# Kernel optimization log

Measured on AMD Instinct MI355X. Metric: run time of the kernel, lower is better.

Reference implementation:

```python
import jax, jax.numpy as jnp
import numpy as np

D_MODEL = 1024
N_HEADS = 16
D_K = D_MODEL // N_HEADS


def setup_inputs() -> dict:
    key = jax.random.key(0)
    ks = jax.random.split(key, 5)
    s = 1.0 / np.sqrt(D_MODEL)
    x = jax.random.normal(ks[0], (4, 2048, D_MODEL), dtype=jnp.float32)
    W_qkv = jax.random.normal(ks[1], (D_MODEL, 3 * D_MODEL), dtype=jnp.float32) * s
    b_qkv = jnp.zeros((3 * D_MODEL,), dtype=jnp.float32)
    W_proj = jax.random.normal(ks[2], (D_MODEL, D_MODEL), dtype=jnp.float32) * s
    b_proj = jnp.zeros((D_MODEL,), dtype=jnp.float32)
    return {"x": x, "W_qkv": W_qkv, "b_qkv": b_qkv, "W_proj": W_proj, "b_proj": b_proj}


def reference(x, W_qkv, b_qkv, W_proj, b_proj):
    B, T, C = x.shape
    qkv = x @ W_qkv + b_qkv  # [B,T,3C]
    q, k, v = jnp.split(qkv, 3, axis=2)
    # [B,T,C] -> [B,H,T,dk]
    def to_heads(t):
        return t.reshape(B, T, N_HEADS, D_K).transpose(0, 2, 1, 3)
    q, k, v = to_heads(q), to_heads(k), to_heads(v)
    scale = 1.0 / np.sqrt(D_K)
    att = jnp.einsum('bhqd,bhkd->bhqk', q, k) * scale
    causal = jnp.tril(jnp.ones((T, T), dtype=bool))
    att = jnp.where(causal, att, -jnp.inf)
    att = jax.nn.softmax(att, axis=-1)
    y = jnp.einsum('bhqk,bhkd->bhqd', att, v)
    y = y.transpose(0, 2, 1, 3).reshape(B, T, C)
    return y @ W_proj + b_proj
```

## Files before the change

kernel.cpp:

```cpp
#include <hip/hip_runtime.h>
#include <stdint.h>


typedef float  floatx4  __attribute__((ext_vector_type(4)));
typedef float  f32x16   __attribute__((ext_vector_type(16)));
typedef __bf16 bf16x8   __attribute__((ext_vector_type(8)));
typedef __bf16 bf16x4   __attribute__((ext_vector_type(4)));
typedef unsigned int u32;
typedef u32    u32x4    __attribute__((ext_vector_type(4)));

#define AS1 __attribute__((address_space(1)))
#define AS3 __attribute__((address_space(3)))

__device__ __forceinline__ void gload_lds16(const void* g, void* l) {
    __builtin_amdgcn_global_load_lds((AS1 void*)(uintptr_t)g,
                                     (AS3 void*)(uintptr_t)l, 16, 0, 0);
}

#if __has_builtin(__builtin_amdgcn_exp2f)
#define EXP2F(x) __builtin_amdgcn_exp2f(x)
#else
#define EXP2F(x) exp2f(x)
#endif

__device__ __forceinline__ u32 pkbf(float lo, float hi) {
    union { __bf16 h[2]; u32 u; } x;
    x.h[0] = (__bf16)lo; x.h[1] = (__bf16)hi;
    return x.u;
}

__device__ __forceinline__ void plswap(u32& a, u32& b) {
    asm volatile("v_permlane32_swap_b32 %0, %1" : "+v"(a), "+v"(b));
}

#define LOG2E 1.44269504088896340736f
#define ATT_SC (0.125f * LOG2E)
#define MASK_NEG (-3.0e4f)

static constexpr int Bn = 4, Tn = 2048, Cn = 1024, Hn = 16, DKn = 64;
static constexpr int BT = Bn * Tn;
static constexpr int N_QKV = 3 * Cn;
static constexpr int KPAD = 66;
static constexpr int VPAD = 130;


__global__ void cast_x_kernel(const float* __restrict__ x, __bf16* __restrict__ xb, int n) {
    int i = (blockIdx.x * blockDim.x + threadIdx.x) * 4;
    if (i < n) {
        float4 v = *(const float4*)(x + i);
        bf16x4 o;
        o[0] = (__bf16)v.x; o[1] = (__bf16)v.y; o[2] = (__bf16)v.z; o[3] = (__bf16)v.w;
        *(bf16x4*)(xb + i) = o;
    }
}

__global__ void transpose_cast_kernel(const float* __restrict__ W, __bf16* __restrict__ WT,
                                      int R, int C) {
    __shared__ float tile[32][33];
    int tx = threadIdx.x & 31, ty = threadIdx.x >> 5;
    int r0 = blockIdx.y * 32, c0 = blockIdx.x * 32;
#pragma unroll
    for (int i = 0; i < 4; i++)
        tile[ty + i * 8][tx] = W[(size_t)(r0 + ty + i * 8) * C + c0 + tx];
    __syncthreads();
#pragma unroll
    for (int i = 0; i < 4; i++)
        WT[(size_t)(c0 + ty + i * 8) * R + r0 + tx] = (__bf16)tile[tx][ty + i * 8];
}

__device__ __forceinline__ void xcd_swizzle(int gx, int* bn, int* bm) {
    int flat = blockIdx.y * gx + blockIdx.x;
    int nwg = gx * gridDim.y;
    int cpx = nwg >> 3;
    int swz = (flat & 7) * cpx + (flat >> 3);
    *bm = swz / gx;
    *bn = swz - *bm * gx;
}

__global__ __launch_bounds__(256) void gemm_qkv_kernel(
    const __bf16* __restrict__ A, const __bf16* __restrict__ Bt,
    const float* __restrict__ bias,
    __bf16* __restrict__ Qo, __bf16* __restrict__ Ko, __bf16* __restrict__ Vo) {
    const int K = 1024;
    __shared__ __bf16 Al[128 * 64];
    __shared__ __bf16 Bl[128 * 64];
    int tid = threadIdx.x, w = tid >> 6, lane = tid & 63;
    int lq = lane >> 4, l16 = lane & 15;
    int bm, bn;
    xcd_swizzle(gridDim.x, &bn, &bm);
    int wm = w & 1, wn = w >> 1;

    int srow = lane >> 3;
    int scb  = (lane & 7) ^ (srow & 7);
    const __bf16* Ag = A + (size_t)(bm * 128 + w * 32 + srow) * K + scb * 8;
    const __bf16* Bg = Bt + (size_t)(bn * 128 + w * 32 + srow) * K + scb * 8;
    __bf16* AlW = Al + w * 32 * 64;
    __bf16* BlW = Bl + w * 32 * 64;

    const int co0 = ((0 * 4 + lq) ^ (l16 & 7)) * 8;
    const int co1 = ((1 * 4 + lq) ^ (l16 & 7)) * 8;

    floatx4 acc[4][4] = {};
    for (int k0 = 0; k0 < K; k0 += 64) {
        __syncthreads();
#pragma unroll
        for (int c = 0; c < 4; c++) {
            gload_lds16(Ag + k0 + (size_t)c * 8 * K, AlW + c * 8 * 64);
            gload_lds16(Bg + k0 + (size_t)c * 8 * K, BlW + c * 8 * 64);
        }
        __syncthreads();
#pragma unroll
        for (int ks = 0; ks < 2; ks++) {
            const int co = ks ? co1 : co0;
            bf16x8 af[4], bf[4];
#pragma unroll
            for (int i = 0; i < 4; i++)
                af[i] = *(const bf16x8*)&Al[(wm * 64 + i * 16 + l16) * 64 + co];
#pragma unroll
            for (int i = 0; i < 4; i++)
                bf[i] = *(const bf16x8*)&Bl[(wn * 64 + i * 16 + l16) * 64 + co];
#pragma unroll
            for (int mt = 0; mt < 4; mt++)
#pragma unroll
                for (int nt = 0; nt < 4; nt++)
                    acc[mt][nt] = __builtin_amdgcn_mfma_f32_16x16x32_bf16(
                        af[mt], bf[nt], acc[mt][nt], 0, 0, 0);
        }
    }
#pragma unroll
    for (int nt = 0; nt < 4; nt++) {
        int gbase = bn * 128 + wn * 64 + nt * 16;
        int gcol = gbase + l16;
        int which = gbase >> 10;
        float bv = bias[gcol];
        if (which == 2) {
            int hh = (gbase - 2048) >> 6;
            int dd = ((gbase - 2048) & 63) + l16;
#pragma unroll
            for (int mt = 0; mt < 4; mt++) {
                int growb = bm * 128 + wm * 64 + mt * 16 + lq * 4;
                int bb = growb >> 11, tt = growb & 2047;
                bf16x4 v4;
#pragma unroll
                for (int r = 0; r < 4; r++) v4[r] = (__bf16)(acc[mt][nt][r] + bv);
                *(bf16x4*)&Vo[((size_t)(bb * 16 + hh) * 64 + dd) * 2048 + tt] = v4;
            }
        } else {
            int rem = gbase & 1023;
            int hh = rem >> 6, dd = (rem & 63) + l16;
            __bf16* dst = (which == 0) ? Qo : Ko;
            float scl = (which == 0) ? ATT_SC : 1.0f;
#pragma unroll
            for (int mt = 0; mt < 4; mt++) {
#pragma unroll
                for (int r = 0; r < 4; r++) {
                    int grow = bm * 128 + wm * 64 + mt * 16 + lq * 4 + r;
                    int bb = grow >> 11, tt = grow & 2047;
                    dst[((size_t)(bb * 16 + hh) * 2048 + tt) * 64 + dd] =
                        (__bf16)((acc[mt][nt][r] + bv) * scl);
                }
            }
        }
    }
}

__global__ __launch_bounds__(256) void gemm_proj_kernel(
    const __bf16* __restrict__ A, const __bf16* __restrict__ Bt,
    const float* __restrict__ bias, float* __restrict__ out) {
    const int K = 1024;
    __shared__ __bf16 Al[128 * 64];
    __shared__ __bf16 Bl[128 * 64];
    int tid = threadIdx.x, w = tid >> 6, lane = tid & 63;
    int lq = lane >> 4, l16 = lane & 15;
    int bm, bn;
    xcd_swizzle(gridDim.x, &bn, &bm);
    int wm = w & 1, wn = w >> 1;

    int srow = lane >> 3;
    int scb  = (lane & 7) ^ (srow & 7);
    const __bf16* Ag = A + (size_t)(bm * 128 + w * 32 + srow) * K + scb * 8;
    const __bf16* Bg = Bt + (size_t)(bn * 128 + w * 32 + srow) * K + scb * 8;
    __bf16* AlW = Al + w * 32 * 64;
    __bf16* BlW = Bl + w * 32 * 64;

    const int co0 = ((0 * 4 + lq) ^ (l16 & 7)) * 8;
    const int co1 = ((1 * 4 + lq) ^ (l16 & 7)) * 8;

    floatx4 acc[4][4] = {};
    for (int k0 = 0; k0 < K; k0 += 64) {
        __syncthreads();
#pragma unroll
        for (int c = 0; c < 4; c++) {
            gload_lds16(Ag + k0 + (size_t)c * 8 * K, AlW + c * 8 * 64);
            gload_lds16(Bg + k0 + (size_t)c * 8 * K, BlW + c * 8 * 64);
        }
        __syncthreads();
#pragma unroll
        for (int ks = 0; ks < 2; ks++) {
            const int co = ks ? co1 : co0;
            bf16x8 af[4], bf[4];
#pragma unroll
            for (int i = 0; i < 4; i++)
                af[i] = *(const bf16x8*)&Al[(wm * 64 + i * 16 + l16) * 64 + co];
#pragma unroll
            for (int i = 0; i < 4; i++)
                bf[i] = *(const bf16x8*)&Bl[(wn * 64 + i * 16 + l16) * 64 + co];
#pragma unroll
            for (int mt = 0; mt < 4; mt++)
#pragma unroll
                for (int nt = 0; nt < 4; nt++)
                    acc[mt][nt] = __builtin_amdgcn_mfma_f32_16x16x32_bf16(
                        af[mt], bf[nt], acc[mt][nt], 0, 0, 0);
        }
    }
#pragma unroll
    for (int nt = 0; nt < 4; nt++) {
        int gcol = bn * 128 + wn * 64 + nt * 16 + l16;
        float bv = bias[gcol];
#pragma unroll
        for (int mt = 0; mt < 4; mt++) {
#pragma unroll
            for (int r = 0; r < 4; r++) {
                int grow = bm * 128 + wm * 64 + mt * 16 + lq * 4 + r;
                out[(size_t)grow * 1024 + gcol] = acc[mt][nt][r] + bv;
            }
        }
    }
}

__global__ __launch_bounds__(256) void attn_kernel(
    const __bf16* __restrict__ Q, const __bf16* __restrict__ K,
    const __bf16* __restrict__ Vt, __bf16* __restrict__ Y) {
    const int bid = blockIdx.x;
    const int pr = bid >> 6, bh = bid & 63;
    const int b = bh >> 4, h = bh & 15;
    int tid = threadIdx.x, w = tid >> 6, lane = tid & 63;
    int l32 = lane & 31, hi = lane >> 5;

    const __bf16* Qh = Q + (size_t)bh * Tn * DKn;
    const __bf16* Kh = K + (size_t)bh * Tn * DKn;
    const __bf16* Vh = Vt + (size_t)bh * DKn * Tn;

    __shared__ __bf16 Kl[128 * KPAD];
    __shared__ __bf16 Vl[64 * VPAD];

    int skrow = tid >> 3, sksl = tid & 7;
    int svrow = tid >> 4, svsl = tid & 15;

    bf16x8 kr[4], vr[4];
#pragma unroll
    for (int i = 0; i < 4; i++) {
        kr[i] = *(const bf16x8*)&Kh[(size_t)(skrow + i * 32) * 64 + sksl * 8];
        vr[i] = *(const bf16x8*)&Vh[(size_t)(svrow + i * 16) * 2048 + svsl * 8];
    }

#pragma unroll
    for (int seg = 0; seg < 2; seg++) {
        const int qt = seg ? (15 - pr) : pr;
        const int q0 = qt * 128;
        const int ktmax = qt;
        const int qrow = q0 + w * 32 + l32;

        bf16x8 qf[4];
#pragma unroll
        for (int ds = 0; ds < 4; ds++)
            qf[ds] = *(const bf16x8*)&Qh[(size_t)qrow * 64 + ds * 16 + hi * 8];

        f32x16 oacc0 = {}, oacc1 = {};
        float rs = 0.0f;

        for (int kt = 0; kt <= ktmax; kt++) {
            __syncthreads();
#pragma unroll
            for (int i = 0; i < 4; i++) {
                *(bf16x8*)&Kl[(skrow + i * 32) * KPAD + sksl * 8] = kr[i];
                *(bf16x8*)&Vl[(svrow + i * 16) * VPAD + svsl * 8] = vr[i];
            }
            __syncthreads();
            if (!(seg == 1 && kt == ktmax)) {
                int nk = (kt < ktmax) ? (kt + 1) : 0;
#pragma unroll
                for (int i = 0; i < 4; i++) {
                    kr[i] = *(const bf16x8*)&Kh[(size_t)(nk * 128 + skrow + i * 32) * 64 + sksl * 8];
                    vr[i] = *(const bf16x8*)&Vh[(size_t)(svrow + i * 16) * 2048 + nk * 128 + svsl * 8];
                }
            }

#pragma unroll
            for (int ktile = 0; ktile < 4; ktile++) {
                f32x16 s = {};
#pragma unroll
                for (int ds = 0; ds < 4; ds++) {
                    bf16x8 ka = *(const bf16x8*)&Kl[(ktile * 32 + l32) * KPAD +
                                                    ds * 16 + hi * 8];
                    s = __builtin_amdgcn_mfma_f32_32x32x16_bf16(ka, qf[ds], s, 0, 0, 0);
                }

                if (kt == qt) {
                    int kbase = kt * 128 + ktile * 32 + 4 * hi;
#pragma unroll
                    for (int r = 0; r < 16; r++) {
                        int key = kbase + (r & 3) + 8 * (r >> 2);
                        if (key > qrow) s[r] = MASK_NEG;
                    }
                }

                u32 G0a, G0b, G1a, G1b, G2a, G2b, G3a, G3b;
                {
                    float p0 = EXP2F(s[0]),  p1 = EXP2F(s[1]),  p2 = EXP2F(s[2]),  p3 = EXP2F(s[3]);
                    float p4 = EXP2F(s[4]),  p5 = EXP2F(s[5]),  p6 = EXP2F(s[6]),  p7 = EXP2F(s[7]);
                    float p8 = EXP2F(s[8]),  p9 = EXP2F(s[9]),  pa = EXP2F(s[10]), pb_ = EXP2F(s[11]);
                    float pc = EXP2F(s[12]), pd = EXP2F(s[13]), pe = EXP2F(s[14]), pf = EXP2F(s[15]);
                    rs += (((p0 + p1) + (p2 + p3)) + ((p4 + p5) + (p6 + p7))) +
                          (((p8 + p9) + (pa + pb_)) + ((pc + pd) + (pe + pf)));
                    G0a = pkbf(p0, p1);  G0b = pkbf(p2, p3);
                    G1a = pkbf(p4, p5);  G1b = pkbf(p6, p7);
                    G2a = pkbf(p8, p9);  G2b = pkbf(pa, pb_);
                    G3a = pkbf(pc, pd);  G3b = pkbf(pe, pf);
                }

#pragma unroll
                for (int t = 0; t < 2; t++) {
                    u32 a0 = t ? G2a : G0a, b0 = t ? G3a : G1a;
                    u32 a1 = t ? G2b : G0b, b1 = t ? G3b : G1b;
                    plswap(a0, b0);
                    plswap(a1, b1);
                    u32x4 wv = {a0, a1, b0, b1};
                    bf16x8 pbf = __builtin_bit_cast(bf16x8, wv);

                    int kc = ktile * 32 + t * 16 + hi * 8;
                    bf16x8 va0 = *(const bf16x8*)&Vl[(0 * 32 + l32) * VPAD + kc];
                    bf16x8 va1 = *(const bf16x8*)&Vl[(1 * 32 + l32) * VPAD + kc];
                    oacc0 = __builtin_amdgcn_mfma_f32_32x32x16_bf16(va0, pbf, oacc0, 0, 0, 0);
                    oacc1 = __builtin_amdgcn_mfma_f32_32x32x16_bf16(va1, pbf, oacc1, 0, 0, 0);
                }
            }
        }

        float tot = rs + __shfl_xor(rs, 32);
        float inv = 1.0f / tot;
#pragma unroll
        for (int dt2 = 0; dt2 < 2; dt2++) {
#pragma unroll
            for (int rg = 0; rg < 4; rg++) {
                bf16x4 v4;
#pragma unroll
                for (int e = 0; e < 4; e++) {
                    float o = dt2 ? oacc1[rg * 4 + e] : oacc0[rg * 4 + e];
                    v4[e] = (__bf16)(o * inv);
                }
                int d = dt2 * 32 + 8 * rg + 4 * hi;
                *(bf16x4*)&Y[((size_t)(b * 2048 + qrow)) * 1024 + h * 64 + d] = v4;
            }
        }
    }
}


extern "C" void kernel_launch(void* const* d_in, const int* in_sizes, int n_in,
                              void* d_out, int out_size, void* d_ws, size_t ws_size,
                              hipStream_t stream) {
    const float* x     = (const float*)d_in[0];
    const float* Wqkv  = (const float*)d_in[1];
    const float* bqkv  = (const float*)d_in[2];
    const float* Wproj = (const float*)d_in[3];
    const float* bproj = (const float*)d_in[4];
    float* out = (float*)d_out;

    __bf16* xb     = (__bf16*)d_ws;
    __bf16* WqkvT  = xb + (size_t)BT * Cn;
    __bf16* WprojT = WqkvT + (size_t)N_QKV * Cn;
    __bf16* Qb     = WprojT + (size_t)Cn * Cn;
    __bf16* Kb     = Qb + (size_t)BT * Cn;
    __bf16* Vb     = Kb + (size_t)BT * Cn;
    __bf16* Yb     = Vb + (size_t)BT * Cn;

    int nx = BT * Cn;
    cast_x_kernel<<<(nx / 4 + 255) / 256, 256, 0, stream>>>(x, xb, nx);
    transpose_cast_kernel<<<dim3(N_QKV / 32, Cn / 32), 256, 0, stream>>>(Wqkv, WqkvT, Cn, N_QKV);
    transpose_cast_kernel<<<dim3(Cn / 32, Cn / 32), 256, 0, stream>>>(Wproj, WprojT, Cn, Cn);

    gemm_qkv_kernel<<<dim3(N_QKV / 128, BT / 128), 256, 0, stream>>>(
        xb, WqkvT, bqkv, Qb, Kb, Vb);

    attn_kernel<<<dim3(512), 256, 0, stream>>>(Qb, Kb, Vb, Yb);

    gemm_proj_kernel<<<dim3(Cn / 128, BT / 128), 256, 0, stream>>>(
        Yb, WprojT, bproj, out);
}
```

Before: 247.0 us.

## Process both paired causal query tiles in one shared K/V pass

```diff
diff --git a/kernel.cpp b/kernel.cpp
--- a/kernel.cpp
+++ b/kernel.cpp
@@ -247,6 +247,21 @@
     int skrow = tid >> 3, sksl = tid & 7;
     int svrow = tid >> 4, svsl = tid & 15;
 
+    const int qtA = pr, qtB = 15 - pr;
+    const int NT = qtB + 1;
+    const int qrowA = qtA * 128 + w * 32 + l32;
+    const int qrowB = qtB * 128 + w * 32 + l32;
+
+    bf16x8 qfA[4], qfB[4];
+#pragma unroll
+    for (int ds = 0; ds < 4; ds++) {
+        qfA[ds] = *(const bf16x8*)&Qh[(size_t)qrowA * 64 + ds * 16 + hi * 8];
+        qfB[ds] = *(const bf16x8*)&Qh[(size_t)qrowB * 64 + ds * 16 + hi * 8];
+    }
+
+    f32x16 oA0 = {}, oA1 = {}, oB0 = {}, oB1 = {};
+    float rsA = 0.0f, rsB = 0.0f;
+
     bf16x8 kr[4], vr[4];
 #pragma unroll
     for (int i = 0; i < 4; i++) {
@@ -254,90 +269,122 @@
         vr[i] = *(const bf16x8*)&Vh[(size_t)(svrow + i * 16) * 2048 + svsl * 8];
     }
 
-#pragma unroll
-    for (int seg = 0; seg < 2; seg++) {
-        const int qt = seg ? (15 - pr) : pr;
-        const int q0 = qt * 128;
-        const int ktmax = qt;
-        const int qrow = q0 + w * 32 + l32;
-
-        bf16x8 qf[4];
-#pragma unroll
-        for (int ds = 0; ds < 4; ds++)
-            qf[ds] = *(const bf16x8*)&Qh[(size_t)qrow * 64 + ds * 16 + hi * 8];
-
-        f32x16 oacc0 = {}, oacc1 = {};
-        float rs = 0.0f;
-
-        for (int kt = 0; kt <= ktmax; kt++) {
-            __syncthreads();
+    for (int kt = 0; kt < NT; kt++) {
+        __syncthreads();
+#pragma unroll
+        for (int i = 0; i < 4; i++) {
+            *(bf16x8*)&Kl[(skrow + i * 32) * KPAD + sksl * 8] = kr[i];
+            *(bf16x8*)&Vl[(svrow + i * 16) * VPAD + svsl * 8] = vr[i];
+        }
+        __syncthreads();
+        if (kt + 1 < NT) {
+            int nk = kt + 1;
 #pragma unroll
             for (int i = 0; i < 4; i++) {
-                *(bf16x8*)&Kl[(skrow + i * 32) * KPAD + sksl * 8] = kr[i];
-                *(bf16x8*)&Vl[(svrow + i * 16) * VPAD + svsl * 8] = vr[i];
-            }
-            __syncthreads();
-            if (!(seg == 1 && kt == ktmax)) {
-                int nk = (kt < ktmax) ? (kt + 1) : 0;
-#pragma unroll
-                for (int i = 0; i < 4; i++) {
-                    kr[i] = *(const bf16x8*)&Kh[(size_t)(nk * 128 + skrow + i * 32) * 64 + sksl * 8];
-                    vr[i] = *(const bf16x8*)&Vh[(size_t)(svrow + i * 16) * 2048 + nk * 128 + svsl * 8];
-                }
-            }
-
-#pragma unroll
-            for (int ktile = 0; ktile < 4; ktile++) {
-                f32x16 s = {};
-#pragma unroll
-                for (int ds = 0; ds < 4; ds++) {
-                    bf16x8 ka = *(const bf16x8*)&Kl[(ktile * 32 + l32) * KPAD +
-                                                    ds * 16 + hi * 8];
-                    s = __builtin_amdgcn_mfma_f32_32x32x16_bf16(ka, qf[ds], s, 0, 0, 0);
-                }
-
-                if (kt == qt) {
-                    int kbase = kt * 128 + ktile * 32 + 4 * hi;
-#pragma unroll
-                    for (int r = 0; r < 16; r++) {
-                        int key = kbase + (r & 3) + 8 * (r >> 2);
-                        if (key > qrow) s[r] = MASK_NEG;
-                    }
-                }
-
-                u32 G0a, G0b, G1a, G1b, G2a, G2b, G3a, G3b;
+                kr[i] = *(const bf16x8*)&Kh[(size_t)(nk * 128 + skrow + i * 32) * 64 + sksl * 8];
+                vr[i] = *(const bf16x8*)&Vh[(size_t)(svrow + i * 16) * 2048 + nk * 128 + svsl * 8];
+            }
+        }
+
+        const bool doA = (kt <= qtA);
+        const int kb = kt * 128;
+
+#pragma unroll
+        for (int ktile = 0; ktile < 4; ktile++) {
+            bf16x8 ka4[4];
+#pragma unroll
+            for (int ds = 0; ds < 4; ds++)
+                ka4[ds] = *(const bf16x8*)&Kl[(ktile * 32 + l32) * KPAD + ds * 16 + hi * 8];
+
+            f32x16 sB = {};
+#pragma unroll
+            for (int ds = 0; ds < 4; ds++)
+                sB = __builtin_amdgcn_mfma_f32_32x32x16_bf16(ka4[ds], qfB[ds], sB, 0, 0, 0);
+            f32x16 sA = {};
+            if (doA) {
+#pragma unroll
+                for (int ds = 0; ds < 4; ds++)
+                    sA = __builtin_amdgcn_mfma_f32_32x32x16_bf16(ka4[ds], qfA[ds], sA, 0, 0, 0);
+            }
+
+            if (kt == qtB) {
+                int kbase = kb + ktile * 32 + 4 * hi;
+#pragma unroll
+                for (int r = 0; r < 16; r++) {
+                    int key = kbase + (r & 3) + 8 * (r >> 2);
+                    if (key > qrowB) sB[r] = MASK_NEG;
+                }
+            }
+            if (doA && kt == qtA) {
+                int kbase = kb + ktile * 32 + 4 * hi;
+#pragma unroll
+                for (int r = 0; r < 16; r++) {
+                    int key = kbase + (r & 3) + 8 * (r >> 2);
+                    if (key > qrowA) sA[r] = MASK_NEG;
+                }
+            }
+
+            u32 B0a, B0b, B1a, B1b, B2a, B2b, B3a, B3b;
+            {
+                float p0 = EXP2F(sB[0]),  p1 = EXP2F(sB[1]),  p2 = EXP2F(sB[2]),  p3 = EXP2F(sB[3]);
+                float p4 = EXP2F(sB[4]),  p5 = EXP2F(sB[5]),  p6 = EXP2F(sB[6]),  p7 = EXP2F(sB[7]);
+                float p8 = EXP2F(sB[8]),  p9 = EXP2F(sB[9]),  pa = EXP2F(sB[10]), pb_ = EXP2F(sB[11]);
+                float pc = EXP2F(sB[12]), pd = EXP2F(sB[13]), pe = EXP2F(sB[14]), pf = EXP2F(sB[15]);
+                rsB += (((p0 + p1) + (p2 + p3)) + ((p4 + p5) + (p6 + p7))) +
+                       (((p8 + p9) + (pa + pb_)) + ((pc + pd) + (pe + pf)));
+                B0a = pkbf(p0, p1);  B0b = pkbf(p2, p3);
+                B1a = pkbf(p4, p5);  B1b = pkbf(p6, p7);
+                B2a = pkbf(p8, p9);  B2b = pkbf(pa, pb_);
+                B3a = pkbf(pc, pd);  B3b = pkbf(pe, pf);
+            }
+            u32 A0a, A0b, A1a, A1b, A2a, A2b, A3a, A3b;
+            if (doA) {
+                float p0 = EXP2F(sA[0]),  p1 = EXP2F(sA[1]),  p2 = EXP2F(sA[2]),  p3 = EXP2F(sA[3]);
+                float p4 = EXP2F(sA[4]),  p5 = EXP2F(sA[5]),  p6 = EXP2F(sA[6]),  p7 = EXP2F(sA[7]);
+                float p8 = EXP2F(sA[8]),  p9 = EXP2F(sA[9]),  pa = EXP2F(sA[10]), pb_ = EXP2F(sA[11]);
+                float pc = EXP2F(sA[12]), pd = EXP2F(sA[13]), pe = EXP2F(sA[14]), pf = EXP2F(sA[15]);
+                rsA += (((p0 + p1) + (p2 + p3)) + ((p4 + p5) + (p6 + p7))) +
+                       (((p8 + p9) + (pa + pb_)) + ((pc + pd) + (pe + pf)));
+                A0a = pkbf(p0, p1);  A0b = pkbf(p2, p3);
+                A1a = pkbf(p4, p5);  A1b = pkbf(p6, p7);
+                A2a = pkbf(p8, p9);  A2b = pkbf(pa, pb_);
+                A3a = pkbf(pc, pd);  A3b = pkbf(pe, pf);
+            }
+
+#pragma unroll
+            for (int t = 0; t < 2; t++) {
+                int kc = kb + ktile * 32 + t * 16 + hi * 8;
+                int kcl = ktile * 32 + t * 16 + hi * 8;
+                bf16x8 va0 = *(const bf16x8*)&Vl[(0 * 32 + l32) * VPAD + kcl];
+                bf16x8 va1 = *(const bf16x8*)&Vl[(1 * 32 + l32) * VPAD + kcl];
+                (void)kc;
+
                 {
-                    float p0 = EXP2F(s[0]),  p1 = EXP2F(s[1]),  p2 = EXP2F(s[2]),  p3 = EXP2F(s[3]);
-                    float p4 = EXP2F(s[4]),  p5 = EXP2F(s[5]),  p6 = EXP2F(s[6]),  p7 = EXP2F(s[7]);
-                    float p8 = EXP2F(s[8]),  p9 = EXP2F(s[9]),  pa = EXP2F(s[10]), pb_ = EXP2F(s[11]);
-                    float pc = EXP2F(s[12]), pd = EXP2F(s[13]), pe = EXP2F(s[14]), pf = EXP2F(s[15]);
-                    rs += (((p0 + p1) + (p2 + p3)) + ((p4 + p5) + (p6 + p7))) +
-                          (((p8 + p9) + (pa + pb_)) + ((pc + pd) + (pe + pf)));
-                    G0a = pkbf(p0, p1);  G0b = pkbf(p2, p3);
-                    G1a = pkbf(p4, p5);  G1b = pkbf(p6, p7);
-                    G2a = pkbf(p8, p9);  G2b = pkbf(pa, pb_);
-                    G3a = pkbf(pc, pd);  G3b = pkbf(pe, pf);
-                }
-
-#pragma unroll
-                for (int t = 0; t < 2; t++) {
-                    u32 a0 = t ? G2a : G0a, b0 = t ? G3a : G1a;
-                    u32 a1 = t ? G2b : G0b, b1 = t ? G3b : G1b;
+                    u32 a0 = t ? B2a : B0a, b0 = t ? B3a : B1a;
+                    u32 a1 = t ? B2b : B0b, b1 = t ? B3b : B1b;
                     plswap(a0, b0);
                     plswap(a1, b1);
                     u32x4 wv = {a0, a1, b0, b1};
                     bf16x8 pbf = __builtin_bit_cast(bf16x8, wv);
-
-                    int kc = ktile * 32 + t * 16 + hi * 8;
-                    bf16x8 va0 = *(const bf16x8*)&Vl[(0 * 32 + l32) * VPAD + kc];
-                    bf16x8 va1 = *(const bf16x8*)&Vl[(1 * 32 + l32) * VPAD + kc];
-                    oacc0 = __builtin_amdgcn_mfma_f32_32x32x16_bf16(va0, pbf, oacc0, 0, 0, 0);
-                    oacc1 = __builtin_amdgcn_mfma_f32_32x32x16_bf16(va1, pbf, oacc1, 0, 0, 0);
-                }
-            }
-        }
-
-        float tot = rs + __shfl_xor(rs, 32);
+                    oB0 = __builtin_amdgcn_mfma_f32_32x32x16_bf16(va0, pbf, oB0, 0, 0, 0);
+                    oB1 = __builtin_amdgcn_mfma_f32_32x32x16_bf16(va1, pbf, oB1, 0, 0, 0);
+                }
+                if (doA) {
+                    u32 a0 = t ? A2a : A0a, b0 = t ? A3a : A1a;
+                    u32 a1 = t ? A2b : A0b, b1 = t ? A3b : A1b;
+                    plswap(a0, b0);
+                    plswap(a1, b1);
+                    u32x4 wv = {a0, a1, b0, b1};
+                    bf16x8 pbf = __builtin_bit_cast(bf16x8, wv);
+                    oA0 = __builtin_amdgcn_mfma_f32_32x32x16_bf16(va0, pbf, oA0, 0, 0, 0);
+                    oA1 = __builtin_amdgcn_mfma_f32_32x32x16_bf16(va1, pbf, oA1, 0, 0, 0);
+                }
+            }
+        }
+    }
+
+    {
+        float tot = rsA + __shfl_xor(rsA, 32);
         float inv = 1.0f / tot;
 #pragma unroll
         for (int dt2 = 0; dt2 < 2; dt2++) {
@@ -346,11 +393,29 @@
                 bf16x4 v4;
 #pragma unroll
                 for (int e = 0; e < 4; e++) {
-                    float o = dt2 ? oacc1[rg * 4 + e] : oacc0[rg * 4 + e];
+                    float o = dt2 ? oA1[rg * 4 + e] : oA0[rg * 4 + e];
                     v4[e] = (__bf16)(o * inv);
                 }
                 int d = dt2 * 32 + 8 * rg + 4 * hi;
-                *(bf16x4*)&Y[((size_t)(b * 2048 + qrow)) * 1024 + h * 64 + d] = v4;
+                *(bf16x4*)&Y[((size_t)(b * 2048 + qrowA)) * 1024 + h * 64 + d] = v4;
+            }
+        }
+    }
+    {
+        float tot = rsB + __shfl_xor(rsB, 32);
+        float inv = 1.0f / tot;
+#pragma unroll
+        for (int dt2 = 0; dt2 < 2; dt2++) {
+#pragma unroll
+            for (int rg = 0; rg < 4; rg++) {
+                bf16x4 v4;
+#pragma unroll
+                for (int e = 0; e < 4; e++) {
+                    float o = dt2 ? oB1[rg * 4 + e] : oB0[rg * 4 + e];
+                    v4[e] = (__bf16)(o * inv);
+                }
+                int d = dt2 * 32 + 8 * rg + 4 * hi;
+                *(bf16x4*)&Y[((size_t)(b * 2048 + qrowB)) * 1024 + h * 64 + d] = v4;
             }
         }
     }
```

New measurement: 266.0 us. 7.7% more time.
